# Performance work log

Measured on AMD Instinct MI355X. Metric: run time of the kernel, lower is better.

The kernel has to match this reference:

```python
import jax, jax.numpy as jnp
import numpy as np

# Paul Kellet pink-noise filter coefficients (verbatim from the torch source)
_A = np.array([0.99886, 0.99332, 0.969, 0.8665, 0.55, -0.7616], dtype=np.float32)   # pole feedback
_C = np.array([0.0555179, 0.0750759, 0.153852, 0.3104856, 0.5329522, -0.016898], dtype=np.float32)  # input gains
_B6_GAIN = 0.115926   # b6 is the previous white sample scaled (one-sample delay)
_DIRECT = 0.5362      # direct white feedthrough
_OUT_GAIN = 0.11


def setup_inputs() -> dict:
    key = jax.random.key(0)
    B, L = 256, 65536
    white = jax.random.normal(key, (B, L), dtype=jnp.float32)
    return {"white": white}


def reference(white):
    """Pink noise via the 6-pole IIR recurrence from SignalGenerator.noise('pink'),
    vectorized over a batch of channels; sequential time handled by lax.scan.
    white: [B, L] -> pink: [B, L]
    """
    B, L = white.shape
    a = jnp.asarray(_A)  # [6]
    c = jnp.asarray(_C)  # [6]

    def step(carry, w_t):
        # carry: (b [B,6] pole states, b6 [B] delayed-white state); w_t: [B]
        b, b6 = carry
        b = a * b + w_t[:, None] * c                      # [B,6]
        pink_t = (b.sum(-1) + b6 + _DIRECT * w_t) * _OUT_GAIN  # [B]
        return (b, _B6_GAIN * w_t), pink_t

    init = (jnp.zeros((B, 6), dtype=white.dtype), jnp.zeros((B,), dtype=white.dtype))
    _, pink_tb = jax.lax.scan(step, init, white.T)  # scan over time: [L, B]
    return pink_tb.T  # [B, L]
```

## Files before the change

kernel.cpp:

```cpp
#include <hip/hip_runtime.h>


constexpr int kL = 65536;
constexpr int kThr = 512;
constexpr int kWaves = kThr / 64;
constexpr int kHalf = kThr / 2;
constexpr int kT = 8192;
constexpr int kW = 8192;
constexpr int kPT = 32;
constexpr int kTilesPerCh = kL / kT;

__device__ __forceinline__ int swz(int i) {
    return i ^ (((i >> 5) & 7) << 2);
}

__global__ __launch_bounds__(kThr, 3) void pink_tile(
    const float* __restrict__ white, float* __restrict__ pink)
{
    constexpr float A[6] = {0.99886f, 0.99332f, 0.969f, 0.8665f, 0.55f, -0.7616f};
    constexpr float C[6] = {0.0555179f, 0.0750759f, 0.153852f, 0.3104856f, 0.5329522f, -0.016898f};
    constexpr float B6G = 0.115926f, DIRECT = 0.5362f, OUTG = 0.11f;

    __shared__ __align__(16) float buf[kT];
    __shared__ float swv[6][kWaves];

    const int tid = threadIdx.x, lane = tid & 63, wave = tid >> 6;
    const int ch = blockIdx.x / kTilesPerCh;
    const int tI = blockIdx.x % kTilesPerCh;
    const size_t outBase = (size_t)ch * kL + (size_t)tI * kT;

    float mPT[6], pmL[6], Mwv[6];
    #pragma unroll
    for (int p = 0; p < 6; ++p) {
        float q = A[p];
        #pragma unroll
        for (int i = 0; i < 5; ++i) q *= q;
        mPT[p] = q;
        float pm = 1.f, qq = q;
        #pragma unroll
        for (int b = 0; b < 6; ++b) { if ((lane >> b) & 1) pm *= qq; qq *= qq; }
        pmL[p] = pm;
        Mwv[p] = qq;
    }

    float e[6] = {0.f, 0.f, 0.f, 0.f, 0.f, 0.f};

    if (tid < kHalf) {
        if (tI != 0) {
            const float* g = white + outBase - kW + (size_t)kPT * tid;
            #pragma unroll
            for (int kk = 0; kk < kPT / 4; ++kk) {
                const float4 x = *(const float4*)(g + 4 * kk);
                const float* xp = &x.x;
                #pragma unroll
                for (int j = 0; j < 4; ++j) {
                    const float ww = xp[j];
                    #pragma unroll
                    for (int p = 0; p < 6; ++p) e[p] = fmaf(A[p], e[p], ww * C[p]);
                }
            }
        }
    } else {
        const int u = tid - kHalf;
        const float4* src4 = (const float4*)(white + outBase);
        #pragma unroll
        for (int g2 = 0; g2 < 2; ++g2) {
            float4 v[4];
            #pragma unroll
            for (int k = 0; k < 4; ++k) v[k] = src4[u + (g2 * 4 + k) * kHalf];
            #pragma unroll
            for (int k = 0; k < 4; ++k)
                *(float4*)&buf[swz(4 * (u + (g2 * 4 + k) * kHalf))] = v[k];
        }
    }
    __syncthreads();

    float pwl = 0.f;
    if (tid >= kHalf) {
        const int u = tid - kHalf;
        #pragma unroll
        for (int kk = 0; kk < kPT / 4; ++kk) {
            const float4 x = *(const float4*)&buf[swz(kPT * u + 4 * kk)];
            const float* xp = &x.x;
            #pragma unroll
            for (int j = 0; j < 4; ++j) {
                const float ww = xp[j];
                #pragma unroll
                for (int p = 0; p < 6; ++p) e[p] = fmaf(A[p], e[p], ww * C[p]);
            }
        }
        if (u == 0) pwl = (tI != 0) ? white[outBase - 1] : 0.f;
        else        pwl = buf[swz(kPT * u - 1)];
    }

    float mk[6];
    #pragma unroll
    for (int p = 0; p < 6; ++p) mk[p] = mPT[p];
    #pragma unroll
    for (int r = 0; r < 6; ++r) {
        const int off = 1 << r;
        float fe[6];
        #pragma unroll
        for (int p = 0; p < 6; ++p) fe[p] = __shfl_up(e[p], off);
        if (lane >= off) {
            #pragma unroll
            for (int p = 0; p < 6; ++p) e[p] = fmaf(mk[p], fe[p], e[p]);
        }
        #pragma unroll
        for (int p = 0; p < 6; ++p) mk[p] *= mk[p];
    }
    float ex[6];
    #pragma unroll
    for (int p = 0; p < 6; ++p) {
        ex[p] = __shfl_up(e[p], 1);
        if (lane == 0) ex[p] = 0.f;
    }
    if (lane == 63) {
        #pragma unroll
        for (int p = 0; p < 6; ++p) swv[p][wave] = e[p];
    }
    __syncthreads();

    if (tid >= kHalf) {
        const int u = tid - kHalf;
        float b[6];
        #pragma unroll
        for (int p = 0; p < 6; ++p) {
            float X = 0.f;
            #pragma unroll
            for (int w2 = 0; w2 < kWaves; ++w2)
                if (w2 < wave) X = fmaf(Mwv[p], X, swv[p][w2]);
            b[p] = fmaf(pmL[p], X, ex[p]);
        }
        float b6 = B6G * pwl;
        #pragma unroll
        for (int kk = 0; kk < kPT / 4; ++kk) {
            const float4 x = *(const float4*)&buf[swz(kPT * u + 4 * kk)];
            const float* xp = &x.x;
            float4 o;
            float* op = &o.x;
            #pragma unroll
            for (int j = 0; j < 4; ++j) {
                const float ww = xp[j];
                #pragma unroll
                for (int p = 0; p < 6; ++p) b[p] = fmaf(A[p], b[p], ww * C[p]);
                const float sum = ((b[0]+b[1]) + (b[2]+b[3])) + ((b[4]+b[5]) + b6);
                op[j] = fmaf(DIRECT, ww, sum) * OUTG;
                b6 = B6G * ww;
            }
            *(float4*)&buf[swz(kPT * u + 4 * kk)] = o;
        }
    }
    __syncthreads();

    float4* dst4 = (float4*)(pink + outBase);
    #pragma unroll
    for (int k = 0; k < 4; ++k)
        dst4[tid + k * kThr] = *(const float4*)&buf[swz(4 * (tid + k * kThr))];
}

extern "C" void kernel_launch(void* const* d_in, const int* in_sizes, int n_in,
                              void* d_out, int out_size, void* d_ws, size_t ws_size,
                              hipStream_t stream) {
    const float* white = (const float*)d_in[0];
    float* pink = (float*)d_out;
    const int nCh = in_sizes[0] / kL;
    const int nBlk = nCh * kTilesPerCh;

    hipLaunchKernelGGL(pink_tile, dim3(nBlk), dim3(kThr), 0, stream,
                       white, pink);
}
```

Before: 127.4 us.

## Use all threads for warmup and main scan instead of splitting block halves

Previously half the block ran a 32-sample warmup recurrence over the previous window while the other half loaded the tile. Both then waited on the busy half, so the later phases ran on only half the threads. Now all 512 threads run the warmup window at 16 samples each, do a wave/block scan, and fold the result into a carry. The full block then processes the current tile with the same scan. This halves the per-thread sequential chain length but adds a second shuffle scan and extra barriers.

```diff
diff --git a/kernel.cpp b/kernel.cpp
--- a/kernel.cpp
+++ b/kernel.cpp
@@ -4,10 +4,9 @@
 constexpr int kL = 65536;
 constexpr int kThr = 512;
 constexpr int kWaves = kThr / 64;
-constexpr int kHalf = kThr / 2;
 constexpr int kT = 8192;
 constexpr int kW = 8192;
-constexpr int kPT = 32;
+constexpr int kPT = kT / kThr;
 constexpr int kTilesPerCh = kL / kT;
 
 __device__ __forceinline__ int swz(int i) {
@@ -29,12 +28,15 @@
     const int tI = blockIdx.x % kTilesPerCh;
     const size_t outBase = (size_t)ch * kL + (size_t)tI * kT;
 
+    float pw0 = 0.f;
+    if (tid == 0 && tI != 0) pw0 = white[outBase - 1];
+
     float mPT[6], pmL[6], Mwv[6];
     #pragma unroll
     for (int p = 0; p < 6; ++p) {
         float q = A[p];
         #pragma unroll
-        for (int i = 0; i < 5; ++i) q *= q;
+        for (int i = 0; i < 4; ++i) q *= q;
         mPT[p] = q;
         float pm = 1.f, qq = q;
         #pragma unroll
@@ -43,44 +45,27 @@
         Mwv[p] = qq;
     }
 
-    float e[6] = {0.f, 0.f, 0.f, 0.f, 0.f, 0.f};
-
-    if (tid < kHalf) {
-        if (tI != 0) {
-            const float* g = white + outBase - kW + (size_t)kPT * tid;
-            #pragma unroll
-            for (int kk = 0; kk < kPT / 4; ++kk) {
-                const float4 x = *(const float4*)(g + 4 * kk);
-                const float* xp = &x.x;
-                #pragma unroll
-                for (int j = 0; j < 4; ++j) {
-                    const float ww = xp[j];
-                    #pragma unroll
-                    for (int p = 0; p < 6; ++p) e[p] = fmaf(A[p], e[p], ww * C[p]);
-                }
-            }
-        }
-    } else {
-        const int u = tid - kHalf;
-        const float4* src4 = (const float4*)(white + outBase);
-        #pragma unroll
-        for (int g2 = 0; g2 < 2; ++g2) {
-            float4 v[4];
-            #pragma unroll
-            for (int k = 0; k < 4; ++k) v[k] = src4[u + (g2 * 4 + k) * kHalf];
-            #pragma unroll
-            for (int k = 0; k < 4; ++k)
-                *(float4*)&buf[swz(4 * (u + (g2 * 4 + k) * kHalf))] = v[k];
-        }
-    }
-    __syncthreads();
-
-    float pwl = 0.f;
-    if (tid >= kHalf) {
-        const int u = tid - kHalf;
+    float R[6] = {0.f, 0.f, 0.f, 0.f, 0.f, 0.f};
+
+    const float4* srcB = (const float4*)(white + outBase);
+    float4 vB[4];
+
+    if (tI != 0) {
+        const float4* srcA = (const float4*)(white + outBase - kW);
+        float4 vA[4];
+        #pragma unroll
+        for (int k = 0; k < 4; ++k) vA[k] = srcA[tid + k * kThr];
+        #pragma unroll
+        for (int k = 0; k < 4; ++k) vB[k] = srcB[tid + k * kThr];
+        #pragma unroll
+        for (int k = 0; k < 4; ++k)
+            *(float4*)&buf[swz(4 * (tid + k * kThr))] = vA[k];
+        __syncthreads();
+
+        float e[6] = {0.f, 0.f, 0.f, 0.f, 0.f, 0.f};
         #pragma unroll
         for (int kk = 0; kk < kPT / 4; ++kk) {
-            const float4 x = *(const float4*)&buf[swz(kPT * u + 4 * kk)];
+            const float4 x = *(const float4*)&buf[swz(kPT * tid + 4 * kk)];
             const float* xp = &x.x;
             #pragma unroll
             for (int j = 0; j < 4; ++j) {
@@ -89,9 +74,56 @@
                 for (int p = 0; p < 6; ++p) e[p] = fmaf(A[p], e[p], ww * C[p]);
             }
         }
-        if (u == 0) pwl = (tI != 0) ? white[outBase - 1] : 0.f;
-        else        pwl = buf[swz(kPT * u - 1)];
-    }
+        float mk[6];
+        #pragma unroll
+        for (int p = 0; p < 6; ++p) mk[p] = mPT[p];
+        #pragma unroll
+        for (int r = 0; r < 6; ++r) {
+            const int off = 1 << r;
+            float fe[6];
+            #pragma unroll
+            for (int p = 0; p < 6; ++p) fe[p] = __shfl_up(e[p], off);
+            if (lane >= off) {
+                #pragma unroll
+                for (int p = 0; p < 6; ++p) e[p] = fmaf(mk[p], fe[p], e[p]);
+            }
+            #pragma unroll
+            for (int p = 0; p < 6; ++p) mk[p] *= mk[p];
+        }
+        if (lane == 63) {
+            #pragma unroll
+            for (int p = 0; p < 6; ++p) swv[p][wave] = e[p];
+        }
+        __syncthreads();
+
+        #pragma unroll
+        for (int w2 = 0; w2 < kWaves; ++w2) {
+            #pragma unroll
+            for (int p = 0; p < 6; ++p) R[p] = fmaf(Mwv[p], R[p], swv[p][w2]);
+        }
+    } else {
+        #pragma unroll
+        for (int k = 0; k < 4; ++k) vB[k] = srcB[tid + k * kThr];
+    }
+
+    #pragma unroll
+    for (int k = 0; k < 4; ++k)
+        *(float4*)&buf[swz(4 * (tid + k * kThr))] = vB[k];
+    __syncthreads();
+
+    float e[6] = {0.f, 0.f, 0.f, 0.f, 0.f, 0.f};
+    #pragma unroll
+    for (int kk = 0; kk < kPT / 4; ++kk) {
+        const float4 x = *(const float4*)&buf[swz(kPT * tid + 4 * kk)];
+        const float* xp = &x.x;
+        #pragma unroll
+        for (int j = 0; j < 4; ++j) {
+            const float ww = xp[j];
+            #pragma unroll
+            for (int p = 0; p < 6; ++p) e[p] = fmaf(A[p], e[p], ww * C[p]);
+        }
+    }
+    const float pwl = (tid == 0) ? pw0 : buf[swz(kPT * tid - 1)];
 
     float mk[6];
     #pragma unroll
@@ -121,35 +153,33 @@
     }
     __syncthreads();
 
-    if (tid >= kHalf) {
-        const int u = tid - kHalf;
-        float b[6];
-        #pragma unroll
-        for (int p = 0; p < 6; ++p) {
-            float X = 0.f;
-            #pragma unroll
-            for (int w2 = 0; w2 < kWaves; ++w2)
-                if (w2 < wave) X = fmaf(Mwv[p], X, swv[p][w2]);
-            b[p] = fmaf(pmL[p], X, ex[p]);
-        }
-        float b6 = B6G * pwl;
-        #pragma unroll
-        for (int kk = 0; kk < kPT / 4; ++kk) {
-            const float4 x = *(const float4*)&buf[swz(kPT * u + 4 * kk)];
-            const float* xp = &x.x;
-            float4 o;
-            float* op = &o.x;
-            #pragma unroll
-            for (int j = 0; j < 4; ++j) {
-                const float ww = xp[j];
-                #pragma unroll
-                for (int p = 0; p < 6; ++p) b[p] = fmaf(A[p], b[p], ww * C[p]);
-                const float sum = ((b[0]+b[1]) + (b[2]+b[3])) + ((b[4]+b[5]) + b6);
-                op[j] = fmaf(DIRECT, ww, sum) * OUTG;
-                b6 = B6G * ww;
-            }
-            *(float4*)&buf[swz(kPT * u + 4 * kk)] = o;
-        }
+    float b[6];
+    #pragma unroll
+    for (int p = 0; p < 6; ++p) {
+        float X = R[p];
+        #pragma unroll
+        for (int w2 = 0; w2 < kWaves; ++w2)
+            if (w2 < wave) X = fmaf(Mwv[p], X, swv[p][w2]);
+        b[p] = fmaf(pmL[p], X, ex[p]);
+    }
+    float b6 = B6G * pwl;
+
+    #pragma unroll
+    for (int kk = 0; kk < kPT / 4; ++kk) {
+        const float4 x = *(const float4*)&buf[swz(kPT * tid + 4 * kk)];
+        const float* xp = &x.x;
+        float4 o;
+        float* op = &o.x;
+        #pragma unroll
+        for (int j = 0; j < 4; ++j) {
+            const float ww = xp[j];
+            #pragma unroll
+            for (int p = 0; p < 6; ++p) b[p] = fmaf(A[p], b[p], ww * C[p]);
+            const float sum = ((b[0]+b[1]) + (b[2]+b[3])) + ((b[4]+b[5]) + b6);
+            op[j] = fmaf(DIRECT, ww, sum) * OUTG;
+            b6 = B6G * ww;
+        }
+        *(float4*)&buf[swz(kPT * tid + 4 * kk)] = o;
     }
     __syncthreads();
 
```

Measured after the change: 141.0 us. 10.6% more time.
